# Performance work log

Hardware: AMD Instinct MI355X
Metric: run time of the kernel (lower is better)

Reference implementation:

```python
import jax, jax.numpy as jnp
import numpy as np

B, T, H = 2, 2048, 1024
NH = 16
HD = H // NH


def setup_inputs() -> dict:
    key = jax.random.key(0)
    ks = jax.random.split(key, 9)
    s = 0.02
    return {
        "x": jax.random.normal(ks[0], (B, T, H), dtype=jnp.float32),
        "attn_mask": jnp.ones((B, T), dtype=jnp.int32),
        "Wq": jax.random.normal(ks[1], (H, H), dtype=jnp.float32) * s,
        "bq": jnp.zeros((H,), dtype=jnp.float32),
        "Wk": jax.random.normal(ks[2], (H, H), dtype=jnp.float32) * s,
        "bk": jnp.zeros((H,), dtype=jnp.float32),
        "Wv": jax.random.normal(ks[3], (H, H), dtype=jnp.float32) * s,
        "bv": jnp.zeros((H,), dtype=jnp.float32),
        "Wo": jax.random.normal(ks[4], (H, H), dtype=jnp.float32) * s,
        "bo": jnp.zeros((H,), dtype=jnp.float32),
    }


def reference(x, attn_mask, Wq, bq, Wk, bk, Wv, bv, Wo, bo):
    Bc, Tc, Hc = x.shape
    scale = HD ** -0.5
    # projections; torch Linear: y = x @ W.T + b (here W stored as [in,out])
    q = (x @ Wq + bq).reshape(Bc, Tc, NH, HD).transpose(0, 2, 1, 3)  # [B,NH,T,HD]
    k = (x @ Wk + bk).reshape(Bc, Tc, NH, HD).transpose(0, 2, 1, 3)
    v = (x @ Wv + bv).reshape(Bc, Tc, NH, HD).transpose(0, 2, 1, 3)
    scores = jnp.einsum('bhqd,bhkd->bhqk', q, k) * scale  # [B,NH,T,T]
    mask = attn_mask.reshape(Bc, 1, 1, Tc)
    scores = jnp.where(mask == 0, jnp.float32(-jnp.inf), scores)
    probs = jax.nn.softmax(scores, axis=-1)
    ctx = jnp.einsum('bhqk,bhkd->bhqd', probs, v)  # [B,NH,T,HD]
    ctx = ctx.transpose(0, 2, 1, 3).reshape(Bc, Tc, Hc)
    out = ctx @ Wo + bo
    return out
```

## Files before the change

kernel.cpp:

```cpp
#include <hip/hip_runtime.h>

typedef _Float16 f16;
typedef _Float16 f16x8 __attribute__((ext_vector_type(8)));
typedef _Float16 f16x4 __attribute__((ext_vector_type(4)));
typedef __fp16 h16x2 __attribute__((ext_vector_type(2)));
typedef float f32x4 __attribute__((ext_vector_type(4)));

#define MFMA32(a, b, c) __builtin_amdgcn_mfma_f32_16x16x32_f16((a), (b), (c), 0, 0, 0)

static constexpr int Bb = 2, T = 2048, H = 1024, NH = 16, HD = 64;
static constexpr int M = Bb * T;
static constexpr int NQK = 2 * H;
#define QSCALE 0.1803368801111f

__device__ __forceinline__ void gload_lds16(const void* g, void* l) {
  __builtin_amdgcn_global_load_lds(
      (const __attribute__((address_space(1))) void*)g,
      (__attribute__((address_space(3))) void*)l, 16, 0, 0);
}

__global__ __launch_bounds__(256) void pack_all(const float* __restrict__ x,
                                                const float* __restrict__ Wq,
                                                const float* __restrict__ Wk,
                                                const float* __restrict__ Wv,
                                                const float* __restrict__ Wo,
                                                const float* __restrict__ bq,
                                                const float* __restrict__ bk,
                                                const float* __restrict__ bv,
                                                const int* __restrict__ mask,
                                                f16* __restrict__ xh,
                                                f16* __restrict__ WqkvT,
                                                f16* __restrict__ WoT,
                                                float* __restrict__ bqkv,
                                                float* __restrict__ maskf) {
  __shared__ f16 tile[64][65];
  const int bid = blockIdx.x;
  if (bid < 4096) {
    int i = bid * 256 + threadIdx.x;
    float4 v = ((const float4*)x)[i];
    f16x4 o;
    o[0] = (f16)v.x; o[1] = (f16)v.y; o[2] = (f16)v.z; o[3] = (f16)v.w;
    *(f16x4*)(xh + (size_t)i * 4) = o;
  } else if (bid < 5120) {
    int t = bid - 4096;
    int z = t >> 8, rem = t & 255;
    const float* W = (z == 0) ? Wq : (z == 1) ? Wk : (z == 2) ? Wv : Wo;
    f16* Wt = (z < 3) ? (WqkvT + (size_t)z * H * H) : WoT;
    const float scale = (z == 0) ? QSCALE : 1.0f;
    int k0 = (rem >> 4) * 64, n0 = (rem & 15) * 64;
    for (int p = 0; p < 16; ++p) {
      int idx = threadIdx.x + p * 256;
      int r = idx >> 6, c = idx & 63;
      tile[r][c] = (f16)(W[(size_t)(k0 + r) * H + n0 + c] * scale);
    }
    __syncthreads();
    for (int p = 0; p < 16; ++p) {
      int idx = threadIdx.x + p * 256;
      int r = idx >> 6, c = idx & 63;
      Wt[(size_t)(n0 + r) * H + k0 + c] = tile[c][r];
    }
  } else if (bid < 5132) {
    int i = (bid - 5120) * 256 + threadIdx.x;
    if (i < 3072) {
      float v = (i < 1024) ? bq[i] * QSCALE : ((i < 2048) ? bk[i - 1024] : bv[i - 2048]);
      bqkv[i] = v;
    }
  } else {
    int i = (bid - 5132) * 256 + threadIdx.x;
    if (i < Bb * T) maskf[i] = mask[i] ? 1.0f : 0.0f;
  }
}

__device__ __forceinline__ f16x8 lds_frag(const f16* base, int row, int gr) {
  return *(const f16x8*)(base + row * 64 + ((gr ^ (row & 7)) << 3));
}

__global__ __launch_bounds__(256, 3) void gemm_qkv(const f16* __restrict__ A,
                                                   const f16* __restrict__ Bt,
                                                   const float* __restrict__ bias,
                                                   f16* __restrict__ QK,
                                                   f16* __restrict__ VT) {
  constexpr int TM = 128, TN = 64, Kk = 1024;
  __shared__ f16 As[2][TM * 64];
  __shared__ f16 Bs[2][TN * 64];
  const int tid = threadIdx.x;
  const int lane = tid & 63, w = tid >> 6;
  const int quad = lane >> 4, l16 = lane & 15;
  const int wm = w >> 1, wn = w & 1;
  const int m0 = blockIdx.y * TM, n0 = blockIdx.x * TN;

  f32x4 acc[4][2];
  for (int a = 0; a < 4; ++a)
    for (int b2 = 0; b2 < 2; ++b2)
      for (int r = 0; r < 4; ++r) acc[a][b2][r] = 0.f;

  auto stage = [&](int k0, int buf) {
    for (int p = 0; p < 4; ++p) {
      int slot = p * 256 + w * 64 + lane;
      int r = slot >> 3, g = (slot & 7) ^ (r & 7);
      gload_lds16(A + (size_t)(m0 + r) * Kk + k0 + g * 8,
                  (char*)&As[buf][0] + (p * 256 + w * 64) * 16);
    }
    for (int p = 0; p < 2; ++p) {
      int slot = p * 256 + w * 64 + lane;
      int r = slot >> 3, g = (slot & 7) ^ (r & 7);
      gload_lds16(Bt + (size_t)(n0 + r) * Kk + k0 + g * 8,
                  (char*)&Bs[buf][0] + (p * 256 + w * 64) * 16);
    }
  };

  stage(0, 0);
  __syncthreads();
  for (int it = 0; it < Kk / 64; ++it) {
    const int cur = it & 1;
    if (it + 1 < Kk / 64) stage((it + 1) * 64, cur ^ 1);
    for (int ks = 0; ks < 2; ++ks) {
      f16x8 af[4], bf[2];
      for (int t = 0; t < 4; ++t)
        af[t] = lds_frag(&As[cur][0], wm * 64 + t * 16 + l16, ks * 4 + quad);
      for (int t = 0; t < 2; ++t)
        bf[t] = lds_frag(&Bs[cur][0], wn * 32 + t * 16 + l16, ks * 4 + quad);
      for (int tm = 0; tm < 4; ++tm)
        for (int tn = 0; tn < 2; ++tn)
          acc[tm][tn] = MFMA32(af[tm], bf[tn], acc[tm][tn]);
    }
    __syncthreads();
  }

  if (n0 < 2048) {
    for (int tm = 0; tm < 4; ++tm)
      for (int tn = 0; tn < 2; ++tn) {
        int n = n0 + wn * 32 + tn * 16 + l16;
        float bn = bias[n];
        for (int r = 0; r < 4; ++r) {
          int m = m0 + wm * 64 + tm * 16 + quad * 4 + r;
          QK[(size_t)m * NQK + n] = (f16)(acc[tm][tn][r] + bn);
        }
      }
  } else {
    for (int tm = 0; tm < 4; ++tm)
      for (int tn = 0; tn < 2; ++tn) {
        int ng = n0 + wn * 32 + tn * 16 + l16;
        float bn = bias[ng];
        int n = ng - 2048;
        int h = n >> 6, d = n & 63;
        int mrow = m0 + wm * 64 + tm * 16 + quad * 4;
        int bb = mrow >> 11, t = mrow & 2047;
        int c = (t & ~127) | ((t + 8 * (d & 15)) & 127);
        f16x4 o;
        for (int r = 0; r < 4; ++r) o[r] = (f16)(acc[tm][tn][r] + bn);
        *(f16x4*)(VT + ((size_t)(bb * NH + h) * HD + d) * T + c) = o;
      }
  }
}

__global__ __launch_bounds__(256, 3) void gemm_out(const f16* __restrict__ A,
                                                   const f16* __restrict__ Bt,
                                                   const float* __restrict__ bias,
                                                   float* __restrict__ Cout) {
  constexpr int TM = 128, TN = 64, Kk = 1024, Nn = 1024;
  __shared__ f16 As[2][TM * 64];
  __shared__ f16 Bs[2][TN * 64];
  const int tid = threadIdx.x;
  const int lane = tid & 63, w = tid >> 6;
  const int quad = lane >> 4, l16 = lane & 15;
  const int wm = w >> 1, wn = w & 1;
  const int m0 = blockIdx.y * TM, n0 = blockIdx.x * TN;

  f32x4 acc[4][2];
  for (int a = 0; a < 4; ++a)
    for (int b2 = 0; b2 < 2; ++b2)
      for (int r = 0; r < 4; ++r) acc[a][b2][r] = 0.f;

  auto stage = [&](int k0, int buf) {
    for (int p = 0; p < 4; ++p) {
      int slot = p * 256 + w * 64 + lane;
      int r = slot >> 3, g = (slot & 7) ^ (r & 7);
      gload_lds16(A + (size_t)(m0 + r) * Kk + k0 + g * 8,
                  (char*)&As[buf][0] + (p * 256 + w * 64) * 16);
    }
    for (int p = 0; p < 2; ++p) {
      int slot = p * 256 + w * 64 + lane;
      int r = slot >> 3, g = (slot & 7) ^ (r & 7);
      gload_lds16(Bt + (size_t)(n0 + r) * Kk + k0 + g * 8,
                  (char*)&Bs[buf][0] + (p * 256 + w * 64) * 16);
    }
  };

  stage(0, 0);
  __syncthreads();
  for (int it = 0; it < Kk / 64; ++it) {
    const int cur = it & 1;
    if (it + 1 < Kk / 64) stage((it + 1) * 64, cur ^ 1);
    for (int ks = 0; ks < 2; ++ks) {
      f16x8 af[4], bf[2];
      for (int t = 0; t < 4; ++t)
        af[t] = lds_frag(&As[cur][0], wm * 64 + t * 16 + l16, ks * 4 + quad);
      for (int t = 0; t < 2; ++t)
        bf[t] = lds_frag(&Bs[cur][0], wn * 32 + t * 16 + l16, ks * 4 + quad);
      for (int tm = 0; tm < 4; ++tm)
        for (int tn = 0; tn < 2; ++tn)
          acc[tm][tn] = MFMA32(af[tm], bf[tn], acc[tm][tn]);
    }
    __syncthreads();
  }

  for (int tm = 0; tm < 4; ++tm)
    for (int tn = 0; tn < 2; ++tn) {
      int n = n0 + wn * 32 + tn * 16 + l16;
      float bn = bias[n];
      for (int r = 0; r < 4; ++r) {
        int m = m0 + wm * 64 + tm * 16 + quad * 4 + r;
        Cout[(size_t)m * Nn + n] = acc[tm][tn][r] + bn;
      }
    }
}


static constexpr int KT_ELE = 128 * 64;
static constexpr int VT_ELE = 64 * 128;

__global__ __launch_bounds__(512, 2) void attn_fused(const f16* __restrict__ QK,
                                                     const f16* __restrict__ VT,
                                                     const float* __restrict__ maskf,
                                                     f16* __restrict__ ctx) {
  __shared__ __align__(16) char smem[70656];
  f16* KtB = (f16*)smem;
  f16* VtB = (f16*)(smem + 2 * KT_ELE * 2);

  const int tid = threadIdx.x;
  const int w = tid >> 6, lane = tid & 63;
  const int quad = lane >> 4, l16 = lane & 15;
  const int qw = w & 3, g = w >> 2;
  const int q0 = blockIdx.x * 256, h = blockIdx.y, b = blockIdx.z;

  const size_t kbase = (size_t)(b * T) * NQK + H + h * HD;
  const size_t vtbase = ((size_t)(b * NH + h) * HD) * T;
  const float* maskp = maskf + b * T;

  f16x8 qf[4][2];
  for (int tq = 0; tq < 4; ++tq) {
    const f16* qrow = QK + (size_t)(b * T + q0 + qw * 64 + tq * 16 + l16) * NQK + h * HD;
    qf[tq][0] = *(const f16x8*)(qrow + quad * 8);
    qf[tq][1] = *(const f16x8*)(qrow + 32 + quad * 8);
  }

  f32x4 oacc[4][4];
  float lsum[4] = {0.f, 0.f, 0.f, 0.f};
  for (int tq = 0; tq < 4; ++tq)
    for (int t = 0; t < 4; ++t)
      for (int r = 0; r < 4; ++r) oacc[tq][t][r] = 0.f;

  auto stage = [&](int kv0, int buf) {
    f16* Kd = KtB + buf * KT_ELE;
    f16* Vd = VtB + buf * VT_ELE;
    for (int p = 0; p < 2; ++p) {
      int s = p * 512 + tid;
      int R = s >> 3, sg = (s & 7) ^ (R & 7);
      int kv = (R & ~31) | ((R & 12) << 1) | ((R & 16) >> 2) | (R & 3);
      gload_lds16(QK + kbase + (size_t)(kv0 + kv) * NQK + sg * 8,
                  (char*)Kd + (p * 512 + w * 64) * 16);
    }
    for (int p = 0; p < 2; ++p) {
      int s = p * 512 + tid;
      int d = s >> 4, cg = s & 15;
      gload_lds16(VT + vtbase + (size_t)d * T + kv0 + cg * 8,
                  (char*)Vd + (p * 512 + w * 64) * 16);
    }
  };

  stage(0, 0);
  __syncthreads();

  for (int it = 0; it < T / 128; ++it) {
    const int cur = it & 1;
    if (it + 1 < T / 128) stage((it + 1) * 128, cur ^ 1);

    const f16* Kc = KtB + cur * KT_ELE;
    const f16* Vc = VtB + cur * VT_ELE;

    for (int s = 0; s < 2; ++s) {
      const int bi = g * 2 + s;
      const int kvabs = it * 128 + bi * 32;
      float4 m0 = *(const float4*)(maskp + kvabs + quad * 8);
      float4 m1 = *(const float4*)(maskp + kvabs + quad * 8 + 4);
      f16x8 kfA0 = lds_frag(Kc, bi * 32 + l16, quad);
      f16x8 kfA1 = lds_frag(Kc, bi * 32 + l16, 4 + quad);
      f16x8 kfB0 = lds_frag(Kc, bi * 32 + 16 + l16, quad);
      f16x8 kfB1 = lds_frag(Kc, bi * 32 + 16 + l16, 4 + quad);
      f16x8 vf[4];
      for (int td = 0; td < 4; ++td)
        vf[td] = *(const f16x8*)&Vc[(td * 16 + l16) * 128 +
                                    ((bi * 32 + quad * 8 + 8 * l16) & 127)];

      f32x4 sA[4], sB[4];
      for (int tq = 0; tq < 4; ++tq) {
        f32x4 z = {0.f, 0.f, 0.f, 0.f};
        sA[tq] = MFMA32(kfA0, qf[tq][0], z);
        sB[tq] = MFMA32(kfB0, qf[tq][0], z);
      }
      for (int tq = 0; tq < 4; ++tq) {
        sA[tq] = MFMA32(kfA1, qf[tq][1], sA[tq]);
        sB[tq] = MFMA32(kfB1, qf[tq][1], sB[tq]);
      }

      f16x8 pf[4];
      for (int tq = 0; tq < 4; ++tq) {
        float pA0 = __builtin_amdgcn_exp2f(sA[tq][0]) * m0.x;
        float pA1 = __builtin_amdgcn_exp2f(sA[tq][1]) * m0.y;
        float pA2 = __builtin_amdgcn_exp2f(sA[tq][2]) * m0.z;
        float pA3 = __builtin_amdgcn_exp2f(sA[tq][3]) * m0.w;
        float pB0 = __builtin_amdgcn_exp2f(sB[tq][0]) * m1.x;
        float pB1 = __builtin_amdgcn_exp2f(sB[tq][1]) * m1.y;
        float pB2 = __builtin_amdgcn_exp2f(sB[tq][2]) * m1.z;
        float pB3 = __builtin_amdgcn_exp2f(sB[tq][3]) * m1.w;
        lsum[tq] += ((pA0 + pA1) + (pA2 + pA3)) + ((pB0 + pB1) + (pB2 + pB3));
        union PF { f16x8 v; h16x2 h[4]; } u;
        u.h[0] = __builtin_amdgcn_cvt_pkrtz(pA0, pA1);
        u.h[1] = __builtin_amdgcn_cvt_pkrtz(pA2, pA3);
        u.h[2] = __builtin_amdgcn_cvt_pkrtz(pB0, pB1);
        u.h[3] = __builtin_amdgcn_cvt_pkrtz(pB2, pB3);
        pf[tq] = u.v;
      }

      for (int tq = 0; tq < 4; ++tq)
        for (int td = 0; td < 4; ++td)
          oacc[tq][td] = MFMA32(vf[td], pf[tq], oacc[tq][td]);
    }
    __syncthreads();
  }

  float* cmb = (float*)smem;
  const int slot = qw * 64 + lane;
  if (g == 1) {
    float* dst = cmb + slot * 69;
    int i = 0;
    for (int tq = 0; tq < 4; ++tq)
      for (int td = 0; td < 4; ++td)
        for (int r = 0; r < 4; ++r) dst[i++] = oacc[tq][td][r];
    for (int tq = 0; tq < 4; ++tq) dst[64 + tq] = lsum[tq];
  }
  __syncthreads();
  if (g == 0) {
    const float* src = cmb + slot * 69;
    int i = 0;
    for (int tq = 0; tq < 4; ++tq)
      for (int td = 0; td < 4; ++td)
        for (int r = 0; r < 4; ++r) oacc[tq][td][r] += src[i++];
    for (int tq = 0; tq < 4; ++tq) lsum[tq] += src[64 + tq];

    for (int tq = 0; tq < 4; ++tq) {
      float l = lsum[tq];
      l += __shfl_xor(l, 16, 64);
      l += __shfl_xor(l, 32, 64);
      float inv = 1.f / l;
      int row = b * T + q0 + qw * 64 + tq * 16 + l16;
      for (int td = 0; td < 4; ++td) {
        f16x4 o;
        for (int r = 0; r < 4; ++r) o[r] = (f16)(oacc[tq][td][r] * inv);
        *(f16x4*)(ctx + (size_t)row * H + h * HD + td * 16 + quad * 4) = o;
      }
    }
  }
}


extern "C" void kernel_launch(void* const* d_in, const int* in_sizes, int n_in,
                              void* d_out, int out_size, void* d_ws, size_t ws_size,
                              hipStream_t stream) {
  const float* x  = (const float*)d_in[0];
  const int* mask = (const int*)d_in[1];
  const float* Wq = (const float*)d_in[2];
  const float* bq = (const float*)d_in[3];
  const float* Wk = (const float*)d_in[4];
  const float* bk = (const float*)d_in[5];
  const float* Wv = (const float*)d_in[6];
  const float* bv = (const float*)d_in[7];
  const float* Wo = (const float*)d_in[8];
  const float* bo = (const float*)d_in[9];
  float* out = (float*)d_out;

  char* ws = (char*)d_ws;
  f16* xh      = (f16*)(ws);
  f16* Wqkv_t  = (f16*)(ws + (8u  << 20));
  f16* Wot     = (f16*)(ws + (14u << 20));
  float* bqkv  = (float*)(ws + (16u << 20));
  float* maskf = (float*)(ws + (16u << 20) + 65536);
  f16* QK      = (f16*)(ws + (17u << 20));
  f16* ctx     = (f16*)(ws + (34u << 20));
  f16* VTr     = (f16*)(ws + (43u << 20));

  pack_all<<<dim3(5164), 256, 0, stream>>>(x, Wq, Wk, Wv, Wo, bq, bk, bv, mask,
                                           xh, Wqkv_t, Wot, bqkv, maskf);

  gemm_qkv<<<dim3(3 * H / 64, M / 128), 256, 0, stream>>>(
      xh, Wqkv_t, bqkv, QK, VTr);

  attn_fused<<<dim3(T / 256, NH, Bb), 512, 0, stream>>>(QK, VTr, maskf, ctx);

  gemm_out<<<dim3(H / 64, M / 128), 256, 0, stream>>>(ctx, Wot, bo, out);
}
```

Before: 189.3 us.

## Fold mask into MFMA accumulator, sum probabilities via MFMA, remap blocks per XCD

Result: faster. 184.6 us (-2.5%).

```diff
diff --git a/kernel.cpp b/kernel.cpp
--- a/kernel.cpp
+++ b/kernel.cpp
@@ -67,7 +67,7 @@
     }
   } else {
     int i = (bid - 5132) * 256 + threadIdx.x;
-    if (i < Bb * T) maskf[i] = mask[i] ? 1.0f : 0.0f;
+    if (i < Bb * T) maskf[i] = mask[i] ? 0.0f : -30000.0f;
   }
 }
 
@@ -232,7 +232,13 @@
   const int w = tid >> 6, lane = tid & 63;
   const int quad = lane >> 4, l16 = lane & 15;
   const int qw = w & 3, g = w >> 2;
-  const int q0 = blockIdx.x * 256, h = blockIdx.y, b = blockIdx.z;
+
+  const int flat = blockIdx.x + (T / 256) * (blockIdx.y + NH * blockIdx.z);
+  const int xcd = flat & 7, idx = flat >> 3;
+  const int bh = xcd * 4 + (idx >> 3);
+  const int qb = idx & 7;
+  const int h = bh & 15, b = bh >> 4;
+  const int q0 = qb * 256;
 
   const size_t kbase = (size_t)(b * T) * NQK + H + h * HD;
   const size_t vtbase = ((size_t)(b * NH + h) * HD) * T;
@@ -245,11 +251,16 @@
     qf[tq][1] = *(const f16x8*)(qrow + 32 + quad * 8);
   }
 
+  f16x8 onesf;
+  for (int i = 0; i < 8; ++i) onesf[i] = (f16)1.0f;
+
   f32x4 oacc[4][4];
-  float lsum[4] = {0.f, 0.f, 0.f, 0.f};
-  for (int tq = 0; tq < 4; ++tq)
+  f32x4 lacc[4];
+  for (int tq = 0; tq < 4; ++tq) {
+    for (int r = 0; r < 4; ++r) lacc[tq][r] = 0.f;
     for (int t = 0; t < 4; ++t)
       for (int r = 0; r < 4; ++r) oacc[tq][t][r] = 0.f;
+  }
 
   auto stage = [&](int kv0, int buf) {
     f16* Kd = KtB + buf * KT_ELE;
@@ -284,6 +295,9 @@
       const int kvabs = it * 128 + bi * 32;
       float4 m0 = *(const float4*)(maskp + kvabs + quad * 8);
       float4 m1 = *(const float4*)(maskp + kvabs + quad * 8 + 4);
+      f32x4 zA, zB;
+      zA[0] = m0.x; zA[1] = m0.y; zA[2] = m0.z; zA[3] = m0.w;
+      zB[0] = m1.x; zB[1] = m1.y; zB[2] = m1.z; zB[3] = m1.w;
       f16x8 kfA0 = lds_frag(Kc, bi * 32 + l16, quad);
       f16x8 kfA1 = lds_frag(Kc, bi * 32 + l16, 4 + quad);
       f16x8 kfB0 = lds_frag(Kc, bi * 32 + 16 + l16, quad);
@@ -295,9 +309,8 @@
 
       f32x4 sA[4], sB[4];
       for (int tq = 0; tq < 4; ++tq) {
-        f32x4 z = {0.f, 0.f, 0.f, 0.f};
-        sA[tq] = MFMA32(kfA0, qf[tq][0], z);
-        sB[tq] = MFMA32(kfB0, qf[tq][0], z);
+        sA[tq] = MFMA32(kfA0, qf[tq][0], zA);
+        sB[tq] = MFMA32(kfB0, qf[tq][0], zB);
       }
       for (int tq = 0; tq < 4; ++tq) {
         sA[tq] = MFMA32(kfA1, qf[tq][1], sA[tq]);
@@ -306,15 +319,14 @@
 
       f16x8 pf[4];
       for (int tq = 0; tq < 4; ++tq) {
-        float pA0 = __builtin_amdgcn_exp2f(sA[tq][0]) * m0.x;
-        float pA1 = __builtin_amdgcn_exp2f(sA[tq][1]) * m0.y;
-        float pA2 = __builtin_amdgcn_exp2f(sA[tq][2]) * m0.z;
-        float pA3 = __builtin_amdgcn_exp2f(sA[tq][3]) * m0.w;
-        float pB0 = __builtin_amdgcn_exp2f(sB[tq][0]) * m1.x;
-        float pB1 = __builtin_amdgcn_exp2f(sB[tq][1]) * m1.y;
-        float pB2 = __builtin_amdgcn_exp2f(sB[tq][2]) * m1.z;
-        float pB3 = __builtin_amdgcn_exp2f(sB[tq][3]) * m1.w;
-        lsum[tq] += ((pA0 + pA1) + (pA2 + pA3)) + ((pB0 + pB1) + (pB2 + pB3));
+        float pA0 = __builtin_amdgcn_exp2f(sA[tq][0]);
+        float pA1 = __builtin_amdgcn_exp2f(sA[tq][1]);
+        float pA2 = __builtin_amdgcn_exp2f(sA[tq][2]);
+        float pA3 = __builtin_amdgcn_exp2f(sA[tq][3]);
+        float pB0 = __builtin_amdgcn_exp2f(sB[tq][0]);
+        float pB1 = __builtin_amdgcn_exp2f(sB[tq][1]);
+        float pB2 = __builtin_amdgcn_exp2f(sB[tq][2]);
+        float pB3 = __builtin_amdgcn_exp2f(sB[tq][3]);
         union PF { f16x8 v; h16x2 h[4]; } u;
         u.h[0] = __builtin_amdgcn_cvt_pkrtz(pA0, pA1);
         u.h[1] = __builtin_amdgcn_cvt_pkrtz(pA2, pA3);
@@ -323,9 +335,11 @@
         pf[tq] = u.v;
       }
 
-      for (int tq = 0; tq < 4; ++tq)
+      for (int tq = 0; tq < 4; ++tq) {
         for (int td = 0; td < 4; ++td)
           oacc[tq][td] = MFMA32(vf[td], pf[tq], oacc[tq][td]);
+        lacc[tq] = MFMA32(onesf, pf[tq], lacc[tq]);
+      }
     }
     __syncthreads();
   }
@@ -338,7 +352,7 @@
     for (int tq = 0; tq < 4; ++tq)
       for (int td = 0; td < 4; ++td)
         for (int r = 0; r < 4; ++r) dst[i++] = oacc[tq][td][r];
-    for (int tq = 0; tq < 4; ++tq) dst[64 + tq] = lsum[tq];
+    for (int tq = 0; tq < 4; ++tq) dst[64 + tq] = lacc[tq][0];
   }
   __syncthreads();
   if (g == 0) {
@@ -347,12 +361,9 @@
     for (int tq = 0; tq < 4; ++tq)
       for (int td = 0; td < 4; ++td)
         for (int r = 0; r < 4; ++r) oacc[tq][td][r] += src[i++];
-    for (int tq = 0; tq < 4; ++tq) lsum[tq] += src[64 + tq];
 
     for (int tq = 0; tq < 4; ++tq) {
-      float l = lsum[tq];
-      l += __shfl_xor(l, 16, 64);
-      l += __shfl_xor(l, 32, 64);
+      float l = lacc[tq][0] + src[64 + tq];
       float inv = 1.f / l;
       int row = b * T + q0 + qw * 64 + tq * 16 + l16;
       for (int td = 0; td < 4; ++td) {
```
